# Optimization experiments

Measured on AMD Instinct MI355X. Metric: run time of the kernel, lower is better.

The kernel has to match this reference:

```python
import math
import jax, jax.numpy as jnp
import numpy as np

B, T, D, H, L, DFF = 8, 256, 256, 8, 4, 1024
RBF_DIM = 128
TIME_DIM = D - RBF_DIM  # 128
VOCAB = 64
DH = D // H
RBF_GAP = 0.05
CENTERS = jnp.linspace(0.0, 6.4, RBF_DIM)


def _ln(x, g, b, eps=1e-6):
    m = jnp.mean(x, -1, keepdims=True)
    v = jnp.mean((x - m) ** 2, -1, keepdims=True)
    return (x - m) * jax.lax.rsqrt(v + eps) * g + b


def setup_inputs() -> dict:
    key = jax.random.key(0)
    ks = jax.random.split(key, 24)
    s = 0.02

    def W(k, *shape):
        return jax.random.normal(k, shape, jnp.float32) * s

    emb = W(ks[0], VOCAB, D).at[0].set(0.0)  # padding_idx=0
    return {
        'src': jax.random.randint(ks[1], (B, T), 0, VOCAB),
        'lengths': jax.random.randint(ks[2], (B,), T // 2, T + 1),
        'bond_matrix': jax.random.uniform(ks[3], (B, T, T), jnp.float32, 0.0, 6.4),
        'timestep': jax.random.uniform(ks[4], (B,), jnp.float32, 0.0, 1000.0),
        'emb_table': emb,
        't_w1': W(ks[5], TIME_DIM, TIME_DIM), 't_b1': jnp.zeros((TIME_DIM,), jnp.float32),
        't_w2': W(ks[6], TIME_DIM, TIME_DIM), 't_b2': jnp.zeros((TIME_DIM,), jnp.float32),
        'u': jax.random.normal(ks[7], (D,), jnp.float32) * s,
        'v': jax.random.normal(ks[8], (D,), jnp.float32) * s,
        'Wq': W(ks[9], L, D, D), 'bq': jnp.zeros((L, D), jnp.float32),
        'Wk': W(ks[10], L, D, D), 'bk': jnp.zeros((L, D), jnp.float32),
        'Wv': W(ks[11], L, D, D), 'bv': jnp.zeros((L, D), jnp.float32),
        'Wo': W(ks[12], L, D, D), 'bo': jnp.zeros((L, D), jnp.float32),
        'ln1_g': jnp.ones((L, D), jnp.float32), 'ln1_b': jnp.zeros((L, D), jnp.float32),
        'ln2_g': jnp.ones((L, D), jnp.float32), 'ln2_b': jnp.zeros((L, D), jnp.float32),
        'ff_w1': W(ks[13], L, D, DFF), 'ff_b1': jnp.zeros((L, DFF), jnp.float32),
        'ff_w2': W(ks[14], L, DFF, D), 'ff_b2': jnp.zeros((L, D), jnp.float32),
        'lnf_g': jnp.ones((D,), jnp.float32), 'lnf_b': jnp.zeros((D,), jnp.float32),
    }


def _forward(src, lengths, bond_matrix, timestep, emb_table, t_w1, t_b1, t_w2, t_b2,
             u, v, Wq, bq, Wk, bk, Wv, bv, Wo, bo, ln1_g, ln1_b, ln2_g, ln2_b,
             ff_w1, ff_b1, ff_w2, ff_b2, lnf_g, lnf_b):
    pad = jnp.arange(T) >= lengths[:, None]            # [B,T] True = padding
    pair_mask = pad[:, None, :] | pad[:, :, None]      # [B,T,T]
    # RBF expansion of distances; padded pairs pushed to 1e9 -> rbf ~ 0
    dmat = jnp.where(pair_mask, 1e9, bond_matrix)
    rbf = jnp.exp(-(dmat[..., None] - CENTERS) ** 2 / RBF_GAP)   # [B,T,T,RBF_DIM]
    # sinusoidal timestep embedding -> MLP (Linear, SiLU, Linear)
    half = TIME_DIM // 2
    freqs = jnp.exp(-jnp.log(jnp.asarray(10000.0, jnp.float32)) * jnp.arange(half, dtype=jnp.float32) / half)
    ang = timestep[:, None] * freqs
    temb = jnp.concatenate([jnp.cos(ang), jnp.sin(ang)], -1)
    temb = jax.nn.silu(temb @ t_w1 + t_b1) @ t_w2 + t_b2          # [B,TIME_DIM]
    # pairwise relative embedding: concat(rbf, broadcast time) -> [B,T,T,D]
    rel = jnp.concatenate([rbf, jnp.broadcast_to(temb[:, None, None, :], (B, T, T, TIME_DIM))], -1)
    rel = rel.reshape(B, T, T, H, DH)

    x = emb_table[src]                                  # [B,T,D]
    amask = pad[:, None, None, :]                       # [B,1,1,T]
    uu = u.reshape(H, 1, DH)
    vv = v.reshape(H, 1, DH)
    scale = 1.0 / math.sqrt(DH)

    def step(x, p):
        wq, bq_, wk, bk_, wv, bv_, wo, bo_, g1, b1_, g2, b2_, w1, fb1, w2, fb2 = p
        h = _ln(x, g1, b1_)
        q = (h @ wq + bq_).reshape(B, T, H, DH).transpose(0, 2, 1, 3) * scale
        k = (h @ wk + bk_).reshape(B, T, H, DH).transpose(0, 2, 1, 3)
        val = (h @ wv + bv_).reshape(B, T, H, DH).transpose(0, 2, 1, 3)
        a_c = jnp.einsum('bhqd,bhkd->bhqk', q + uu, k)            # content score
        b_d = jnp.einsum('bhqd,bqkhd->bhqk', q + vv, rel)         # relative-position score
        scores = jnp.where(amask, -1e18, a_c + b_d)
        attn = jax.nn.softmax(scores, -1)
        ctx = jnp.einsum('bhqk,bhkd->bqhd', attn, val).reshape(B, T, D)
        out = ctx @ wo + bo_ + x
        h2 = _ln(out, g2, b2_)
        return jax.nn.relu(h2 @ w1 + fb1) @ w2 + fb2 + out, None

    x, _ = jax.lax.scan(step, x, (Wq, bq, Wk, bk, Wv, bv, Wo, bo,
                                  ln1_g, ln1_b, ln2_g, ln2_b,
                                  ff_w1, ff_b1, ff_w2, ff_b2))
    return _ln(x, lnf_g, lnf_b)


def reference(src, lengths, bond_matrix, timestep, emb_table, t_w1, t_b1, t_w2, t_b2,
              u, v, Wq, bq, Wk, bk, Wv, bv, Wo, bo, ln1_g, ln1_b, ln2_g, ln2_b,
              ff_w1, ff_b1, ff_w2, ff_b2, lnf_g, lnf_b):
    return _forward(src, lengths, bond_matrix, timestep, emb_table, t_w1, t_b1, t_w2, t_b2,
                    u, v, Wq, bq, Wk, bk, Wv, bv, Wo, bo, ln1_g, ln1_b, ln2_g, ln2_b,
                    ff_w1, ff_b1, ff_w2, ff_b2, lnf_g, lnf_b)
```

## Files before the change

kernel.cpp:

```cpp
#include <hip/hip_runtime.h>
#include <hip/hip_bf16.h>
#include <math.h>

#define BB 8
#define TT 256
#define DD 256
#define HH 8
#define DHH 32
#define LL 4
#define DFF 1024
#define QTILE 16

#define RBF_DELTA 0.05039370078740158f
#define RBF_NEGK -28.853900817779268f
#define RBF_M0A 2.9081851339f
#define RBF_M0B -0.0732754690f
#define RBF_RHO 0.9034077526f

typedef __attribute__((ext_vector_type(8))) short short8v;
typedef __attribute__((ext_vector_type(4))) short short4v;
typedef __attribute__((ext_vector_type(4))) float f32x4;

__device__ __forceinline__ ushort f2bf(float x) {
    __hip_bfloat16 h = __float2bfloat16(x);
    return *reinterpret_cast<ushort*>(&h);
}

__global__ void transpose_bf16_kernel(const float* __restrict__ in, ushort* __restrict__ out,
                                      int K, int N, int lstride) {
    __shared__ float tile[32][33];
    int l = blockIdx.z;
    const float* W = in + (size_t)l * lstride;
    ushort* Wt = out + (size_t)l * lstride;
    int kb = blockIdx.y * 32, nb = blockIdx.x * 32;
    int tx = threadIdx.x, ty = threadIdx.y;
#pragma unroll
    for (int i = 0; i < 4; i++) {
        int r = ty + i * 8;
        tile[r][tx] = W[(kb + r) * N + nb + tx];
    }
    __syncthreads();
#pragma unroll
    for (int i = 0; i < 4; i++) {
        int r = ty + i * 8;
        Wt[(nb + r) * K + kb + tx] = f2bf(tile[tx][r]);
    }
}

__global__ void temb_kernel(const float* __restrict__ timestep,
                            const float* __restrict__ t_w1, const float* __restrict__ t_b1,
                            const float* __restrict__ t_w2, const float* __restrict__ t_b2,
                            float* __restrict__ temb_out) {
    __shared__ float s0[128], s1[128];
    int b = blockIdx.x, j = threadIdx.x;
    float ts = timestep[b];
    const float LOG1E4 = 9.210340371976184f;
    if (j < 64) {
        float f = expf(-LOG1E4 * (float)j / 64.f);
        s0[j] = cosf(ts * f);
    } else {
        int i = j - 64;
        float f = expf(-LOG1E4 * (float)i / 64.f);
        s0[j] = sinf(ts * f);
    }
    __syncthreads();
    float acc = t_b1[j];
    for (int i = 0; i < 128; i++) acc += s0[i] * t_w1[i * 128 + j];
    acc = acc / (1.f + expf(-acc));
    s1[j] = acc;
    __syncthreads();
    float acc2 = t_b2[j];
    for (int i = 0; i < 128; i++) acc2 += s1[i] * t_w2[i * 128 + j];
    temb_out[b * 128 + j] = acc2;
}

__global__ void embed_kernel(const int* __restrict__ src, const float* __restrict__ emb,
                             float* __restrict__ x) {
    int r = blockIdx.x, d = threadIdx.x;
    x[r * DD + d] = emb[src[r] * DD + d];
}

template <int OUT_BF16>
__global__ void ln_kernel(const float* __restrict__ in, const float* __restrict__ g,
                          const float* __restrict__ bta, void* __restrict__ out) {
    __shared__ float red[8];
    __shared__ float mv[2];
    int r = blockIdx.x, t = threadIdx.x;
    float v = in[r * DD + t];
    float s = v, s2 = v * v;
    for (int off = 32; off > 0; off >>= 1) {
        s += __shfl_xor(s, off);
        s2 += __shfl_xor(s2, off);
    }
    int w = t >> 6;
    if ((t & 63) == 0) { red[w] = s; red[4 + w] = s2; }
    __syncthreads();
    if (t == 0) {
        float S = red[0] + red[1] + red[2] + red[3];
        float S2 = red[4] + red[5] + red[6] + red[7];
        float m = S * (1.f / 256.f);
        float var = S2 * (1.f / 256.f) - m * m;
        mv[0] = m; mv[1] = rsqrtf(var + 1e-6f);
    }
    __syncthreads();
    float o = (v - mv[0]) * mv[1] * g[t] + bta[t];
    if (OUT_BF16) ((ushort*)out)[r * DD + t] = f2bf(o);
    else          ((float*)out)[r * DD + t] = o;
}

__device__ __forceinline__ void gemm_mfma_body(
    const ushort* __restrict__ A, const ushort* __restrict__ Wt,
    const float* __restrict__ bias, const float* __restrict__ resid,
    void* __restrict__ out, int N, int K, float scale, int RELU, int OUT_BF16) {
    __shared__ __align__(16) ushort smem[10240];
    ushort* As = smem;
    ushort* Bs = smem + 2048;
    float* red = (float*)smem;

    int tid = threadIdx.x;
    int w = tid >> 6, lane = tid & 63;
    int m0 = blockIdx.y * 16, n0 = blockIdx.x * 64;

    f32x4 acc[4] = {f32x4{0,0,0,0}, f32x4{0,0,0,0}, f32x4{0,0,0,0}, f32x4{0,0,0,0}};

    for (int k0 = 0; k0 < K; k0 += 128) {
        {
            int r = tid >> 4, k8 = tid & 15;
            short8v av = *reinterpret_cast<const short8v*>(&A[(m0 + r) * K + k0 + k8 * 8]);
            int dstb = r * 256 + ((k8 * 16) ^ ((r & 7) << 4));
            *reinterpret_cast<short8v*>((char*)As + dstb) = av;
        }
#pragma unroll
        for (int it = 0; it < 4; it++) {
            int idx = it * 256 + tid;
            int r = idx >> 4, k8 = idx & 15;
            short8v bv = *reinterpret_cast<const short8v*>(&Wt[(n0 + r) * K + k0 + k8 * 8]);
            int dstb = r * 256 + ((k8 * 16) ^ ((r & 7) << 4));
            *reinterpret_cast<short8v*>((char*)Bs + dstb) = bv;
        }
        __syncthreads();
        int kb = w * 64 + (lane >> 4) * 16;
        int arow = lane & 15;
        short8v a = *reinterpret_cast<const short8v*>(
            (char*)As + arow * 256 + (kb ^ ((arow & 7) << 4)));
#pragma unroll
        for (int nb = 0; nb < 4; nb++) {
            int nrow = nb * 16 + (lane & 15);
            short8v b = *reinterpret_cast<const short8v*>(
                (char*)Bs + nrow * 256 + (kb ^ ((nrow & 7) << 4)));
            acc[nb] = __builtin_amdgcn_mfma_f32_16x16x32_bf16(a, b, acc[nb], 0, 0, 0);
        }
        __syncthreads();
    }
    if (w > 0) {
        float* r0 = &red[((w - 1) * 64 + lane) * 16];
#pragma unroll
        for (int nb = 0; nb < 4; nb++)
            *reinterpret_cast<f32x4*>(&r0[nb * 4]) = acc[nb];
    }
    __syncthreads();
    if (w == 0) {
        const float* r0 = &red[lane * 16];
        const float* r1 = &red[(64 + lane) * 16];
        const float* r2 = &red[(128 + lane) * 16];
        int col = lane & 15;
#pragma unroll
        for (int nb = 0; nb < 4; nb++) {
            int n = n0 + nb * 16 + col;
            float bia = bias[n];
#pragma unroll
            for (int i = 0; i < 4; i++) {
                int idx = nb * 4 + i;
                int m = m0 + (lane >> 4) * 4 + i;
                float v = acc[nb][i] + r0[idx] + r1[idx] + r2[idx];
                v = (v + bia) * scale;
                if (RELU) v = fmaxf(v, 0.f);
                if (resid) v += resid[m * N + n];
                if (OUT_BF16) ((ushort*)out)[m * N + n] = f2bf(v);
                else          ((float*)out)[m * N + n] = v;
            }
        }
    }
}

template <int RELU, int OUT_BF16>
__global__ __launch_bounds__(256) void gemm_bf16(
    const ushort* __restrict__ A, const ushort* __restrict__ Wt,
    const float* __restrict__ bias, const float* __restrict__ resid,
    void* __restrict__ out, int N, int K, float scale) {
    gemm_mfma_body(A, Wt, bias, resid, out, N, K, scale, RELU, OUT_BF16);
}

__global__ __launch_bounds__(256) void qkv_bf16(
    const ushort* __restrict__ A,
    const ushort* __restrict__ Wqt, const float* __restrict__ bq, float* __restrict__ qo,
    const ushort* __restrict__ Wkt, const float* __restrict__ bk, float* __restrict__ ko,
    const ushort* __restrict__ Wvt, const float* __restrict__ bv, float* __restrict__ vo,
    float qscale) {
    int z = blockIdx.z;
    const ushort* W = (z == 0) ? Wqt : (z == 1) ? Wkt : Wvt;
    const float* bi = (z == 0) ? bq : (z == 1) ? bk : bv;
    float* o = (z == 0) ? qo : (z == 1) ? ko : vo;
    float sc = (z == 0) ? qscale : 1.f;
    gemm_mfma_body(A, W, bi, nullptr, o, DD, DD, sc, 0, 0);
}

__global__ __launch_bounds__(256, 3) void attn_kernel(
    const float* __restrict__ qbuf, const float* __restrict__ kbuf,
    const float* __restrict__ vbuf, const float* __restrict__ u,
    const float* __restrict__ v, const float* __restrict__ temb,
    const float* __restrict__ bond, const int* __restrict__ lengths,
    ushort* __restrict__ ctx) {
    __shared__ float KV[256 * 32];
    __shared__ float sc[QTILE][260];
    __shared__ float qu_s[QTILE][32], qv_s[QTILE][32];
    __shared__ float tq[QTILE];
    __shared__ float temb_s[32];

    int qt = blockIdx.x;
    int h  = blockIdx.y;
    int b  = blockIdx.z;
    int t  = threadIdx.x;
    int len = lengths[b];
    int q0 = qt * QTILE;

    for (int e = t; e < QTILE * 32; e += 256) {
        int q = e >> 5, dh = e & 31;
        float qs = qbuf[(b * TT + q0 + q) * DD + h * 32 + dh];
        qu_s[q][dh] = qs + u[h * 32 + dh];
        qv_s[q][dh] = qs + v[h * 32 + dh];
    }
    if (t < 32) temb_s[t] = (h >= 4) ? temb[b * 128 + (h - 4) * 32 + t] : 0.f;
    for (int e = t; e < 256 * 32; e += 256) {
        int k = e >> 5, dh = e & 31;
        KV[k * 32 + (dh ^ (k & 31))] = kbuf[(b * TT + k) * DD + h * 32 + dh];
    }

    float bond_reg[QTILE];
    if (h < 4) {
        const float* brow = bond + (size_t)(b * TT + q0) * TT + t;
#pragma unroll
        for (int q = 0; q < QTILE; q++) bond_reg[q] = brow[q * TT];
    }
    __syncthreads();

    if (t < QTILE) {
        float a = 0.f;
#pragma unroll
        for (int j = 0; j < 32; j++) a += qv_s[t][j] * temb_s[j];
        tq[t] = a;
    }
    __syncthreads();

    float kreg[32];
    {
        int kx = t & 31;
#pragma unroll
        for (int dh = 0; dh < 32; dh++) kreg[dh] = KV[t * 32 + (dh ^ kx)];
    }

    {
        int k = t;
        bool kvalid = k < len;
        float c0 = (float)(h * 32) * RBF_DELTA;
        for (int q = 0; q < QTILE; q++) {
            float s;
            if (!kvalid) {
                s = -1e18f;
            } else {
                const float* qur = qu_s[q];
                float accA = 0.f;
#pragma unroll
                for (int c = 0; c < 8; c++) {
                    float4 q4 = *reinterpret_cast<const float4*>(&qur[c * 4]);
                    accA = fmaf(q4.x, kreg[c * 4 + 0], accA);
                    accA = fmaf(q4.y, kreg[c * 4 + 1], accA);
                    accA = fmaf(q4.z, kreg[c * 4 + 2], accA);
                    accA = fmaf(q4.w, kreg[c * 4 + 3], accA);
                }
                float accB;
                if (h < 4) {
                    accB = 0.f;
                    if (q0 + q < len) {
                        float diff0 = bond_reg[q] - c0;
                        float tt = exp2f(RBF_NEGK * diff0 * diff0);
                        float m  = exp2f(RBF_M0A * diff0 + RBF_M0B);
                        const float* qvr = qv_s[q];
#pragma unroll
                        for (int c = 0; c < 8; c++) {
                            float4 q4 = *reinterpret_cast<const float4*>(&qvr[c * 4]);
                            accB = fmaf(q4.x, tt, accB); tt *= m; m *= RBF_RHO;
                            accB = fmaf(q4.y, tt, accB); tt *= m; m *= RBF_RHO;
                            accB = fmaf(q4.z, tt, accB); tt *= m; m *= RBF_RHO;
                            accB = fmaf(q4.w, tt, accB); tt *= m; m *= RBF_RHO;
                        }
                    }
                } else {
                    accB = tq[q];
                }
                s = accA + accB;
            }
            sc[q][t] = s;
        }
    }
    __syncthreads();

    {
        int r = t >> 4, j = t & 15;
        float vals[16];
        float mx = -1e30f;
#pragma unroll
        for (int i = 0; i < 16; i++) {
            vals[i] = sc[r][j + 16 * i];
            mx = fmaxf(mx, vals[i]);
        }
        for (int off = 8; off > 0; off >>= 1) mx = fmaxf(mx, __shfl_xor(mx, off));
        float sum = 0.f;
#pragma unroll
        for (int i = 0; i < 16; i++) {
            float e = __expf(vals[i] - mx);
            vals[i] = e; sum += e;
        }
        for (int off = 8; off > 0; off >>= 1) sum += __shfl_xor(sum, off);
        float inv = 1.f / sum;
#pragma unroll
        for (int i = 0; i < 16; i++) sc[r][j + 16 * i] = vals[i] * inv;
    }
    for (int e = t; e < 256 * 32; e += 256) {
        int k2 = e >> 5, dh = e & 31;
        KV[k2 * 32 + (dh ^ (k2 & 31))] = vbuf[(b * TT + k2) * DD + h * 32 + dh];
    }
    __syncthreads();

    {
        int dh = t & 31, qq = t >> 5;
#pragma unroll
        for (int rep = 0; rep < 2; rep++) {
            int q = qq + 8 * rep;
            float acc = 0.f;
#pragma unroll 8
            for (int kk = 0; kk < 256; kk += 4) {
                float4 s4 = *reinterpret_cast<const float4*>(&sc[q][kk]);
                acc = fmaf(s4.x, KV[(kk + 0) * 32 + (dh ^ ((kk + 0) & 31))], acc);
                acc = fmaf(s4.y, KV[(kk + 1) * 32 + (dh ^ ((kk + 1) & 31))], acc);
                acc = fmaf(s4.z, KV[(kk + 2) * 32 + (dh ^ ((kk + 2) & 31))], acc);
                acc = fmaf(s4.w, KV[(kk + 3) * 32 + (dh ^ ((kk + 3) & 31))], acc);
            }
            ctx[(b * TT + q0 + q) * DD + h * 32 + dh] = f2bf(acc);
        }
    }
}

extern "C" void kernel_launch(void* const* d_in, const int* in_sizes, int n_in,
                              void* d_out, int out_size, void* d_ws, size_t ws_size,
                              hipStream_t stream) {
    const int*   src      = (const int*)  d_in[0];
    const int*   lengths  = (const int*)  d_in[1];
    const float* bond     = (const float*)d_in[2];
    const float* timestep = (const float*)d_in[3];
    const float* emb      = (const float*)d_in[4];
    const float* t_w1     = (const float*)d_in[5];
    const float* t_b1     = (const float*)d_in[6];
    const float* t_w2     = (const float*)d_in[7];
    const float* t_b2     = (const float*)d_in[8];
    const float* u        = (const float*)d_in[9];
    const float* v        = (const float*)d_in[10];
    const float* Wq       = (const float*)d_in[11];
    const float* bq       = (const float*)d_in[12];
    const float* Wk       = (const float*)d_in[13];
    const float* bk       = (const float*)d_in[14];
    const float* Wv       = (const float*)d_in[15];
    const float* bv       = (const float*)d_in[16];
    const float* Wo       = (const float*)d_in[17];
    const float* bo       = (const float*)d_in[18];
    const float* ln1_g    = (const float*)d_in[19];
    const float* ln1_b    = (const float*)d_in[20];
    const float* ln2_g    = (const float*)d_in[21];
    const float* ln2_b    = (const float*)d_in[22];
    const float* ff_w1    = (const float*)d_in[23];
    const float* ff_b1    = (const float*)d_in[24];
    const float* ff_w2    = (const float*)d_in[25];
    const float* ff_b2    = (const float*)d_in[26];
    const float* lnf_g    = (const float*)d_in[27];
    const float* lnf_b    = (const float*)d_in[28];

    float* ws   = (float*)d_ws;
    float* xbuf = ws;
    float* qbuf = xbuf + 524288;
    float* kbuf = qbuf + 524288;
    float* vbuf = kbuf + 524288;
    float* obuf = vbuf + 524288;
    float* temb = obuf + 524288;
    ushort* hbuf_bf  = (ushort*)(temb + 1024);
    ushort* cbuf_bf  = hbuf_bf + 524288;
    ushort* ffbuf_bf = cbuf_bf + 524288;
    ushort* wqt_bf   = ffbuf_bf + 2097152;
    ushort* wkt_bf   = wqt_bf + 262144;
    ushort* wvt_bf   = wkt_bf + 262144;
    ushort* wot_bf   = wvt_bf + 262144;
    ushort* ffw1t_bf = wot_bf + 262144;
    ushort* ffw2t_bf = ffw1t_bf + 1048576;

    dim3 tb(32, 8);
    transpose_bf16_kernel<<<dim3(8, 8, 4), tb, 0, stream>>>(Wq, wqt_bf, 256, 256, 65536);
    transpose_bf16_kernel<<<dim3(8, 8, 4), tb, 0, stream>>>(Wk, wkt_bf, 256, 256, 65536);
    transpose_bf16_kernel<<<dim3(8, 8, 4), tb, 0, stream>>>(Wv, wvt_bf, 256, 256, 65536);
    transpose_bf16_kernel<<<dim3(8, 8, 4), tb, 0, stream>>>(Wo, wot_bf, 256, 256, 65536);
    transpose_bf16_kernel<<<dim3(32, 8, 4), tb, 0, stream>>>(ff_w1, ffw1t_bf, 256, 1024, 262144);
    transpose_bf16_kernel<<<dim3(8, 32, 4), tb, 0, stream>>>(ff_w2, ffw2t_bf, 1024, 256, 262144);

    temb_kernel<<<8, 128, 0, stream>>>(timestep, t_w1, t_b1, t_w2, t_b2, temb);
    embed_kernel<<<2048, 256, 0, stream>>>(src, emb, xbuf);

    const float scale = 0.17677669529663687f;
    dim3 gqkv(4, 128, 3);
    dim3 g256(4, 128);
    dim3 g1024(16, 128);

    for (int l = 0; l < LL; l++) {
        ln_kernel<1><<<2048, 256, 0, stream>>>(xbuf, ln1_g + l * 256, ln1_b + l * 256, hbuf_bf);
        qkv_bf16<<<gqkv, 256, 0, stream>>>(hbuf_bf,
            wqt_bf + l * 65536, bq + l * 256, qbuf,
            wkt_bf + l * 65536, bk + l * 256, kbuf,
            wvt_bf + l * 65536, bv + l * 256, vbuf, scale);
        attn_kernel<<<dim3(16, 8, 8), 256, 0, stream>>>(qbuf, kbuf, vbuf, u, v, temb, bond, lengths, cbuf_bf);
        gemm_bf16<0, 0><<<g256, 256, 0, stream>>>(cbuf_bf, wot_bf + l * 65536, bo + l * 256, xbuf, obuf, 256, 256, 1.f);
        ln_kernel<1><<<2048, 256, 0, stream>>>(obuf, ln2_g + l * 256, ln2_b + l * 256, hbuf_bf);
        gemm_bf16<1, 1><<<g1024, 256, 0, stream>>>(hbuf_bf, ffw1t_bf + l * 262144, ff_b1 + l * 1024, nullptr, ffbuf_bf, 1024, 256, 1.f);
        gemm_bf16<0, 0><<<g256, 256, 0, stream>>>(ffbuf_bf, ffw2t_bf + l * 262144, ff_b2 + l * 256, obuf, xbuf, 256, 1024, 1.f);
    }
    ln_kernel<0><<<2048, 256, 0, stream>>>(xbuf, lnf_g, lnf_b, (float*)d_out);
}
```

Measured before the change: 530.4 us.

## Load K directly to registers and stage V as packed bf16 in LDS

The attention kernel now loads each thread's K row straight from global memory into registers with float4 loads, skipping the swizzled LDS staging. V is loaded at the start, converted to packed bf16 pairs, and stored in a half-size LDS buffer, which removes the second global-to-LDS phase after softmax. The PV loop now has each thread compute two output dims with one packed LDS read, and the score loop handles two queries per iteration with split accumulators. Occupancy hint rises from 3 to 4 blocks; V in bf16 adds a small precision loss in the context sum.

```diff
diff --git a/kernel.cpp b/kernel.cpp
--- a/kernel.cpp
+++ b/kernel.cpp
@@ -24,6 +24,9 @@
 __device__ __forceinline__ ushort f2bf(float x) {
     __hip_bfloat16 h = __float2bfloat16(x);
     return *reinterpret_cast<ushort*>(&h);
+}
+__device__ __forceinline__ float bf2f(uint u16) {
+    return __uint_as_float(u16 << 16);
 }
 
 __global__ void transpose_bf16_kernel(const float* __restrict__ in, ushort* __restrict__ out,
@@ -205,13 +208,53 @@
     gemm_mfma_body(A, W, bi, nullptr, o, DD, DD, sc, 0, 0);
 }
 
-__global__ __launch_bounds__(256, 3) void attn_kernel(
+__device__ __forceinline__ float score_one(
+    const float* __restrict__ qur, const float* __restrict__ qvr,
+    const float* kreg, float bondv, float c0, int h, bool qvalid, float tqv) {
+    float a0 = 0.f, a1 = 0.f;
+#pragma unroll
+    for (int c = 0; c < 8; c += 2) {
+        float4 x = *reinterpret_cast<const float4*>(&qur[c * 4]);
+        float4 y = *reinterpret_cast<const float4*>(&qur[c * 4 + 4]);
+        a0 = fmaf(x.x, kreg[c * 4 + 0], a0);
+        a0 = fmaf(x.y, kreg[c * 4 + 1], a0);
+        a0 = fmaf(x.z, kreg[c * 4 + 2], a0);
+        a0 = fmaf(x.w, kreg[c * 4 + 3], a0);
+        a1 = fmaf(y.x, kreg[c * 4 + 4], a1);
+        a1 = fmaf(y.y, kreg[c * 4 + 5], a1);
+        a1 = fmaf(y.z, kreg[c * 4 + 6], a1);
+        a1 = fmaf(y.w, kreg[c * 4 + 7], a1);
+    }
+    float accA = a0 + a1;
+    float accB;
+    if (h < 4) {
+        accB = 0.f;
+        if (qvalid) {
+            float diff0 = bondv - c0;
+            float tt = exp2f(RBF_NEGK * diff0 * diff0);
+            float m  = exp2f(RBF_M0A * diff0 + RBF_M0B);
+#pragma unroll
+            for (int c = 0; c < 8; c++) {
+                float4 q4 = *reinterpret_cast<const float4*>(&qvr[c * 4]);
+                accB = fmaf(q4.x, tt, accB); tt *= m; m *= RBF_RHO;
+                accB = fmaf(q4.y, tt, accB); tt *= m; m *= RBF_RHO;
+                accB = fmaf(q4.z, tt, accB); tt *= m; m *= RBF_RHO;
+                accB = fmaf(q4.w, tt, accB); tt *= m; m *= RBF_RHO;
+            }
+        }
+    } else {
+        accB = tqv;
+    }
+    return accA + accB;
+}
+
+__global__ __launch_bounds__(256, 4) void attn_kernel(
     const float* __restrict__ qbuf, const float* __restrict__ kbuf,
     const float* __restrict__ vbuf, const float* __restrict__ u,
     const float* __restrict__ v, const float* __restrict__ temb,
     const float* __restrict__ bond, const int* __restrict__ lengths,
     ushort* __restrict__ ctx) {
-    __shared__ float KV[256 * 32];
+    __shared__ uint  Vp[256 * 16];
     __shared__ float sc[QTILE][260];
     __shared__ float qu_s[QTILE][32], qv_s[QTILE][32];
     __shared__ float tq[QTILE];
@@ -224,6 +267,23 @@
     int len = lengths[b];
     int q0 = qt * QTILE;
 
+    float kreg[32];
+    {
+        const float* krow = &kbuf[(size_t)(b * TT + t) * DD + h * 32];
+#pragma unroll
+        for (int c = 0; c < 8; c++) {
+            float4 k4 = *reinterpret_cast<const float4*>(&krow[c * 4]);
+            kreg[c * 4 + 0] = k4.x; kreg[c * 4 + 1] = k4.y;
+            kreg[c * 4 + 2] = k4.z; kreg[c * 4 + 3] = k4.w;
+        }
+    }
+    float bond_reg[QTILE];
+    if (h < 4) {
+        const float* brow = bond + (size_t)(b * TT + q0) * TT + t;
+#pragma unroll
+        for (int q = 0; q < QTILE; q++) bond_reg[q] = brow[q * TT];
+    }
+
     for (int e = t; e < QTILE * 32; e += 256) {
         int q = e >> 5, dh = e & 31;
         float qs = qbuf[(b * TT + q0 + q) * DD + h * 32 + dh];
@@ -231,16 +291,12 @@
         qv_s[q][dh] = qs + v[h * 32 + dh];
     }
     if (t < 32) temb_s[t] = (h >= 4) ? temb[b * 128 + (h - 4) * 32 + t] : 0.f;
-    for (int e = t; e < 256 * 32; e += 256) {
-        int k = e >> 5, dh = e & 31;
-        KV[k * 32 + (dh ^ (k & 31))] = kbuf[(b * TT + k) * DD + h * 32 + dh];
-    }
-
-    float bond_reg[QTILE];
-    if (h < 4) {
-        const float* brow = bond + (size_t)(b * TT + q0) * TT + t;
-#pragma unroll
-        for (int q = 0; q < QTILE; q++) bond_reg[q] = brow[q * TT];
+#pragma unroll
+    for (int i = 0; i < 16; i++) {
+        int e = i * 256 + t;
+        int k = e >> 4, dh2 = e & 15;
+        float2 v2 = *reinterpret_cast<const float2*>(&vbuf[(size_t)(b * TT + k) * DD + h * 32 + dh2 * 2]);
+        Vp[e] = (uint)f2bf(v2.x) | ((uint)f2bf(v2.y) << 16);
     }
     __syncthreads();
 
@@ -252,55 +308,19 @@
     }
     __syncthreads();
 
-    float kreg[32];
     {
-        int kx = t & 31;
-#pragma unroll
-        for (int dh = 0; dh < 32; dh++) kreg[dh] = KV[t * 32 + (dh ^ kx)];
-    }
-
-    {
-        int k = t;
-        bool kvalid = k < len;
         float c0 = (float)(h * 32) * RBF_DELTA;
-        for (int q = 0; q < QTILE; q++) {
-            float s;
-            if (!kvalid) {
-                s = -1e18f;
-            } else {
-                const float* qur = qu_s[q];
-                float accA = 0.f;
-#pragma unroll
-                for (int c = 0; c < 8; c++) {
-                    float4 q4 = *reinterpret_cast<const float4*>(&qur[c * 4]);
-                    accA = fmaf(q4.x, kreg[c * 4 + 0], accA);
-                    accA = fmaf(q4.y, kreg[c * 4 + 1], accA);
-                    accA = fmaf(q4.z, kreg[c * 4 + 2], accA);
-                    accA = fmaf(q4.w, kreg[c * 4 + 3], accA);
-                }
-                float accB;
-                if (h < 4) {
-                    accB = 0.f;
-                    if (q0 + q < len) {
-                        float diff0 = bond_reg[q] - c0;
-                        float tt = exp2f(RBF_NEGK * diff0 * diff0);
-                        float m  = exp2f(RBF_M0A * diff0 + RBF_M0B);
-                        const float* qvr = qv_s[q];
-#pragma unroll
-                        for (int c = 0; c < 8; c++) {
-                            float4 q4 = *reinterpret_cast<const float4*>(&qvr[c * 4]);
-                            accB = fmaf(q4.x, tt, accB); tt *= m; m *= RBF_RHO;
-                            accB = fmaf(q4.y, tt, accB); tt *= m; m *= RBF_RHO;
-                            accB = fmaf(q4.z, tt, accB); tt *= m; m *= RBF_RHO;
-                            accB = fmaf(q4.w, tt, accB); tt *= m; m *= RBF_RHO;
-                        }
-                    }
-                } else {
-                    accB = tq[q];
-                }
-                s = accA + accB;
+        if (t >= len) {
+#pragma unroll
+            for (int q = 0; q < QTILE; q++) sc[q][t] = -1e18f;
+        } else {
+            for (int q = 0; q < QTILE; q += 2) {
+                bool qv0 = (q0 + q) < len, qv1 = (q0 + q + 1) < len;
+                float s0 = score_one(qu_s[q],     qv_s[q],     kreg, bond_reg[q],     c0, h, qv0, tq[q]);
+                float s1 = score_one(qu_s[q + 1], qv_s[q + 1], kreg, bond_reg[q + 1], c0, h, qv1, tq[q + 1]);
+                sc[q][t] = s0;
+                sc[q + 1][t] = s1;
             }
-            sc[q][t] = s;
         }
     }
     __syncthreads();
@@ -326,28 +346,31 @@
 #pragma unroll
         for (int i = 0; i < 16; i++) sc[r][j + 16 * i] = vals[i] * inv;
     }
-    for (int e = t; e < 256 * 32; e += 256) {
-        int k2 = e >> 5, dh = e & 31;
-        KV[k2 * 32 + (dh ^ (k2 & 31))] = vbuf[(b * TT + k2) * DD + h * 32 + dh];
-    }
     __syncthreads();
 
     {
-        int dh = t & 31, qq = t >> 5;
-#pragma unroll
-        for (int rep = 0; rep < 2; rep++) {
-            int q = qq + 8 * rep;
-            float acc = 0.f;
+        int dh2 = t & 15, q = t >> 4;
+        float acc0 = 0.f, acc1 = 0.f;
 #pragma unroll 8
-            for (int kk = 0; kk < 256; kk += 4) {
-                float4 s4 = *reinterpret_cast<const float4*>(&sc[q][kk]);
-                acc = fmaf(s4.x, KV[(kk + 0) * 32 + (dh ^ ((kk + 0) & 31))], acc);
-                acc = fmaf(s4.y, KV[(kk + 1) * 32 + (dh ^ ((kk + 1) & 31))], acc);
-                acc = fmaf(s4.z, KV[(kk + 2) * 32 + (dh ^ ((kk + 2) & 31))], acc);
-                acc = fmaf(s4.w, KV[(kk + 3) * 32 + (dh ^ ((kk + 3) & 31))], acc);
-            }
-            ctx[(b * TT + q0 + q) * DD + h * 32 + dh] = f2bf(acc);
-        }
+        for (int kk = 0; kk < 256; kk += 4) {
+            float4 s4 = *reinterpret_cast<const float4*>(&sc[q][kk]);
+            uint p0 = Vp[(kk + 0) * 16 + dh2];
+            uint p1 = Vp[(kk + 1) * 16 + dh2];
+            uint p2 = Vp[(kk + 2) * 16 + dh2];
+            uint p3 = Vp[(kk + 3) * 16 + dh2];
+            acc0 = fmaf(s4.x, bf2f(p0 & 0xffff), acc0);
+            acc1 = fmaf(s4.x, __uint_as_float(p0 & 0xffff0000u), acc1);
+            acc0 = fmaf(s4.y, bf2f(p1 & 0xffff), acc0);
+            acc1 = fmaf(s4.y, __uint_as_float(p1 & 0xffff0000u), acc1);
+            acc0 = fmaf(s4.z, bf2f(p2 & 0xffff), acc0);
+            acc1 = fmaf(s4.z, __uint_as_float(p2 & 0xffff0000u), acc1);
+            acc0 = fmaf(s4.w, bf2f(p3 & 0xffff), acc0);
+            acc1 = fmaf(s4.w, __uint_as_float(p3 & 0xffff0000u), acc1);
+        }
+        ushort2 o;
+        o.x = f2bf(acc0);
+        o.y = f2bf(acc1);
+        *reinterpret_cast<ushort2*>(&ctx[(size_t)(b * TT + q0 + q) * DD + h * 32 + dh2 * 2]) = o;
     }
 }
 
```

After: 526.6 us. About the same (-0.7%).
